# Performance work log

Measured on AMD Instinct MI355X. Metric: run time of the kernel, lower is better.

The kernel has to match this reference:

```python
import jax, jax.numpy as jnp
import numpy as np

B, N, D = 2, 2048, 1536
HEADS, KVH, DQK, DV = 8, 1, 128, 192
G = HEADS // KVH  # query groups per kv head
NP, DP = 512, 128  # pairwise seq len (coarse), pairwise feature dim
SCALE = DQK ** -0.5
CLAMP = 5.0
MOMENTUM = 0.1  # BatchRMSNorm: 1 - 0.9
EPS = 1e-5


def layernorm(x, w, b):
    mu = jnp.mean(x, axis=-1, keepdims=True)
    var = jnp.mean(jnp.square(x - mu), axis=-1, keepdims=True)
    return (x - mu) * jax.lax.rsqrt(var + EPS) * w + b


def setup_inputs() -> dict:
    key = jax.random.key(0)
    ks = jax.random.split(key, 6)
    w = lambda k, shape: jax.random.normal(k, shape, jnp.float32) * 0.02
    return {
        "x": jax.random.normal(ks[0], (B, N, D), jnp.float32),
        "pairwise": jax.random.normal(ks[1], (B, NP, NP, DP), jnp.float32),
        "w_qkv": w(ks[2], (D, HEADS * DQK + KVH * DQK + KVH * DV)),
        "q_w": jnp.ones((DQK,), jnp.float32), "q_b": jnp.zeros((DQK,), jnp.float32),
        "k_w": jnp.ones((DQK,), jnp.float32), "k_b": jnp.zeros((DQK,), jnp.float32),
        "v_w": jnp.ones((DV,), jnp.float32), "v_b": jnp.zeros((DV,), jnp.float32),
        "bias_gamma": jnp.ones((DP,), jnp.float32),
        "bias_beta": jnp.zeros((DP,), jnp.float32),
        "bias_running_var": jnp.ones((DP,), jnp.float32),
        "w_bias": w(ks[3], (DP, HEADS)),
        "w_out": w(ks[4], (HEADS * DV, D)),
        "b_out": jnp.zeros((D,), jnp.float32),
    }


def reference(x, pairwise, w_qkv, q_w, q_b, k_w, k_b, v_w, v_b,
              bias_gamma, bias_beta, bias_running_var, w_bias, w_out, b_out):
    b, n, _ = x.shape
    qkv = x @ w_qkv
    q, k, v = jnp.split(qkv, [HEADS * DQK, HEADS * DQK + KVH * DQK], axis=-1)
    # split heads: q -> b g h n d, k/v -> b h n d
    q = q.reshape(b, n, G, KVH, DQK).transpose(0, 2, 3, 1, 4)
    k = k.reshape(b, n, KVH, DQK).transpose(0, 2, 1, 3)
    v = v.reshape(b, n, KVH, DV).transpose(0, 2, 1, 3)
    q = layernorm(q, q_w, q_b)
    k = layernorm(k, k_w, k_b)
    v = layernorm(v, v_w, v_b)

    sim = jnp.einsum('bghid,bhjd->bghij', q, k) * SCALE

    # BatchRMSNorm (training update of running_var, then normalize)
    flat = pairwise.reshape(-1, DP)
    batch_var = jnp.var(flat, axis=0)  # unbiased=False
    rv = bias_running_var * (1.0 - MOMENTUM) + MOMENTUM * batch_var
    std = jnp.sqrt(rv + EPS)
    normed = pairwise / std * bias_gamma + bias_beta
    bias = jax.nn.gelu(normed, approximate=False) @ w_bias  # b i j (g h)
    bias = bias.reshape(b, NP, NP, G, KVH).transpose(0, 3, 4, 1, 2)  # b g h i j
    r = n // NP  # expand_factor
    bias = jnp.repeat(jnp.repeat(bias, r, axis=-2), r, axis=-1)

    sim = jnp.tanh((sim + bias) / CLAMP) * CLAMP  # softclamp
    attn = jax.nn.softmax(sim, axis=-1)
    out = jnp.einsum('bghij,bhjd->bghid', attn, v)
    out = out.transpose(0, 3, 1, 2, 4).reshape(b, n, HEADS * DV)  # merge heads
    return out @ w_out + b_out
```

## Files before the change

### kernel.cpp

```cpp
#include <hip/hip_runtime.h>
#include <math.h>

typedef _Float16 f16;
typedef unsigned int u32;
typedef __attribute__((ext_vector_type(8))) f16 f16x8;
typedef __attribute__((ext_vector_type(4))) f16 f16x4;
typedef __attribute__((ext_vector_type(4))) float f32x4;
typedef __attribute__((ext_vector_type(16))) float f32x16;

#define DEV static __device__ __forceinline__

#define SEQ 2048
#define DMODEL 1536
#define NHEADS 8
#define DQK 128
#define DVV 192
#define QKVW 1344
#define SCALEQK 0.08838834764831845f
#define LOG2E 1.4426950408889634f

#define OFF_WQKVT 0ull
#define OFF_WOUTT 4128768ull
#define OFF_XH    8847360ull
#define OFF_QKV   21430272ull
#define OFF_Q     43450368ull
#define OFF_K     51838976ull
#define OFF_V     52887552ull
#define OFF_VT    54460416ull
#define OFF_PART  56033280ull
#define OFF_SG    57081856ull
#define OFF_BIASC 57082880ull
#define OFF_AO    65471488ull

DEV float fexp2(float x){
#if __has_builtin(__builtin_amdgcn_exp2f)
  return __builtin_amdgcn_exp2f(x);
#else
  return exp2f(x);
#endif
}
DEV float frcp(float x){
#if __has_builtin(__builtin_amdgcn_rcpf)
  return __builtin_amdgcn_rcpf(x);
#else
  return 1.0f/x;
#endif
}

typedef u32 __attribute__((address_space(1))) u32g;
typedef u32 __attribute__((address_space(3))) u32l;
DEV void g2l16(const void* g, void* l){
  __builtin_amdgcn_global_load_lds((const u32g*)g, (u32l*)l, 16, 0, 0);
}

#define MFMA32(a,b,c) __builtin_amdgcn_mfma_f32_32x32x16_f16(a,b,c,0,0,0)
#define MFMA16(a,b,c) __builtin_amdgcn_mfma_f32_16x16x32_f16(a,b,c,0,0,0)

DEV f32x16 zero16(){
  f32x16 v;
  #pragma unroll
  for (int i=0;i<16;i++) v[i]=0.f;
  return v;
}
DEV f32x4 zero4(){
  f32x4 v;
  #pragma unroll
  for (int i=0;i<4;i++) v[i]=0.f;
  return v;
}

DEV float gelu_f(float x){
  float z  = 0.70710678118654752440f * x;
  float az = fabsf(z);
  float t  = frcp(1.f + 0.3275911f*az);
  float poly = t*(0.254829592f + t*(-0.284496736f + t*(1.421413741f +
               t*(-1.453152027f + t*1.061405429f))));
  float e  = 1.f - poly*fexp2(-z*z*LOG2E);
  float er = (z < 0.f) ? -e : e;
  return 0.5f*x*(1.f + er);
}

__global__ __launch_bounds__(256) void k1_prep(const float* __restrict__ wq, f16* __restrict__ wqT,
                                               const float* __restrict__ wo, f16* __restrict__ woT,
                                               const float* __restrict__ X, f16* __restrict__ Xh){
  __shared__ float t[32][33];
  int bid = blockIdx.x, tid = threadIdx.x;
  if (bid >= 4320){
    size_t i0 = (size_t)(bid - 4320)*2048 + (size_t)tid*8;
    f32x4 a = *(const f32x4*)(X + i0);
    f32x4 b = *(const f32x4*)(X + i0 + 4);
    f16x8 o;
    #pragma unroll
    for (int e=0;e<4;e++){ o[e] = (f16)a[e]; o[4+e] = (f16)b[e]; }
    *(f16x8*)(Xh + i0) = o;
    return;
  }
  int tx = tid & 31, ty = tid >> 5;
  const float* src; f16* dst; int N, x, y;
  if (bid < 2016){ src = wq; dst = wqT; N = 1344; x = bid % 48; y = bid / 48; }
  else { int b2 = bid - 2016; src = wo; dst = woT; N = 1536; x = b2 % 48; y = b2 / 48; }
  int k0 = x*32, n0 = y*32;
  #pragma unroll
  for (int i=0;i<4;i++){ int r = ty+8*i; t[r][tx] = src[(size_t)(k0+r)*N + n0+tx]; }
  __syncthreads();
  #pragma unroll
  for (int i=0;i<4;i++){ int r = ty+8*i; dst[(size_t)(n0+r)*1536 + k0+tx] = (f16)t[tx][r]; }
}

DEV void gemm256_body(const f16* __restrict__ A, const f16* __restrict__ WT,
                      float* __restrict__ C, int ldc, const float* __restrict__ bo,
                      char* lds, int bx, int by, int tid){
  int nb = bx*64, mb = by*256;
  int w = tid>>6, lane = tid&63, li = lane&31, h = lane>>5;
  int srow = lane>>3, sc = lane&7;
  f32x16 acc[2][2];
  acc[0][0]=zero16(); acc[0][1]=zero16(); acc[1][0]=zero16(); acc[1][1]=zero16();

#define G_STAGE(buf, kt_) do { \
    char* ad = lds + (buf)*40960; \
    _Pragma("unroll") \
    for (int s=0;s<8;s++){ \
      int slot = w*8+s; int mlr = slot*8 + srow; int cs = sc ^ (srow&7); \
      g2l16(A + (size_t)(mb+mlr)*DMODEL + (kt_)*64 + cs*8, ad + slot*1024); \
    } \
    char* bd = lds + (buf)*40960 + 32768; \
    _Pragma("unroll") \
    for (int s=0;s<2;s++){ \
      int slot = w*2+s; int nl = slot*8 + srow; int cs = sc ^ (srow&7); \
      g2l16(WT + (size_t)(nb+nl)*DMODEL + (kt_)*64 + cs*8, bd + slot*1024); \
    } } while(0)

  G_STAGE(0,0);
  __syncthreads();
  for (int kt=0; kt<24; kt++){
    int cur = kt&1;
    if (kt<23) G_STAGE(cur^1, kt+1);
    const char* ad = lds + cur*40960;
    const char* bd = lds + cur*40960 + 32768;
    #pragma unroll
    for (int ks=0; ks<4; ks++){
      int cso = ((2*ks+h) ^ (li&7))*16;
      f16x8 a0 = *(const f16x8*)(ad + (w*64      + li)*128 + cso);
      f16x8 a1 = *(const f16x8*)(ad + (w*64 + 32 + li)*128 + cso);
      f16x8 b0 = *(const f16x8*)(bd + (           li)*128 + cso);
      f16x8 b1 = *(const f16x8*)(bd + (      32 + li)*128 + cso);
      acc[0][0] = MFMA32(a0, b0, acc[0][0]);
      acc[0][1] = MFMA32(a0, b1, acc[0][1]);
      acc[1][0] = MFMA32(a1, b0, acc[1][0]);
      acc[1][1] = MFMA32(a1, b1, acc[1][1]);
    }
    __syncthreads();
  }
  float bo0 = bo ? bo[nb+li] : 0.f, bo1 = bo ? bo[nb+32+li] : 0.f;
  #pragma unroll
  for (int mi=0; mi<2; mi++)
    #pragma unroll
    for (int nf=0; nf<2; nf++)
      #pragma unroll
      for (int r=0;r<16;r++){
        int m = mb + w*64 + mi*32 + (r&3) + 8*(r>>2) + 4*h;
        int n = nb + nf*32 + li;
        C[(size_t)m*ldc + n] = acc[mi][nf][r] + (nf ? bo1 : bo0);
      }
#undef G_STAGE
}

DEV void pvar_body(const float* __restrict__ pw, float* __restrict__ partials,
                   char* smem, int id, int tid){
  int q = tid & 31, rg = tid >> 5;
  f32x4 s1 = zero4(), s2 = zero4();
  const float* p0 = pw + ((size_t)id*512 + rg)*128 + q*4;
  #pragma unroll 4
  for (int it=0; it<64; it++){
    f32x4 v = *(const f32x4*)(p0 + (size_t)it*1024);
    s1 += v; s2 += v*v;
  }
  f32x4* r1 = (f32x4*)smem; f32x4* r2 = r1 + 256;
  r1[tid] = s1; r2[tid] = s2;
  __syncthreads();
  if (tid < 64){
    int qq = tid & 31;
    f32x4* rr = (tid >= 32) ? r2 : r1;
    f32x4 a = rr[qq];
    #pragma unroll
    for (int g=1; g<8; g++) a += rr[g*32+qq];
    *(f32x4*)(partials + (size_t)id*256 + ((tid>=32)?128:0) + qq*4) = a;
  }
}

__global__ __launch_bounds__(256,2) void k2_qkv_pvar(const f16* __restrict__ Xh,
    const f16* __restrict__ WT, float* __restrict__ qkv,
    const float* __restrict__ pw, float* __restrict__ partials){
  __shared__ char smem[81920];
  int bid = blockIdx.x, tid = threadIdx.x;
  if (bid % 5 == 0){
    int qid = bid/5;
    int l = (qid&7)*42 + (qid>>3);
    gemm256_body(Xh, WT, qkv, QKVW, (const float*)0, smem, l%21, l/21, tid);
  } else {
    int pid = bid - bid/5 - 1;
    if (pid < 1024) pvar_body(pw, partials, smem, pid, tid);
  }
}

DEV void ln_unit(const float* __restrict__ qkv,
    const float* __restrict__ qw, const float* __restrict__ qb,
    const float* __restrict__ kw, const float* __restrict__ kb,
    const float* __restrict__ vw, const float* __restrict__ vb,
    f16* __restrict__ Q, f16* __restrict__ K, f16* __restrict__ V,
    int unit, int lane){
  int row = unit / 10, seg = unit - row*10;
  int b = row >> 11, n = row & 2047;
  const float* base = qkv + (size_t)row*QKVW;
  if (seg < 9){
    int off = seg*128;
    float x0 = base[off+lane], x1 = base[off+64+lane];
    float s = x0+x1;
    #pragma unroll
    for (int d=32; d>=1; d>>=1) s += __shfl_xor(s, d);
    float mu = s*(1.f/128.f);
    float d0 = x0-mu, d1 = x1-mu;
    float vv = d0*d0 + d1*d1;
    #pragma unroll
    for (int d=32; d>=1; d>>=1) vv += __shfl_xor(vv, d);
    float istd = rsqrtf(vv*(1.f/128.f) + 1e-5f);
    const float* W  = (seg<8)? qw : kw;
    const float* Bi = (seg<8)? qb : kb;
    f16* dst = (seg<8) ? (Q + ((size_t)(b*NHEADS+seg)*SEQ + n)*DQK)
                       : (K + ((size_t)(b*SEQ+n))*DQK);
    dst[lane]    = (f16)(d0*istd*W[lane] + Bi[lane]);
    dst[lane+64] = (f16)(d1*istd*W[lane+64] + Bi[lane+64]);
  } else {
    float x0 = base[1152+lane], x1 = base[1152+64+lane], x2 = base[1152+128+lane];
    float s = x0+x1+x2;
    #pragma unroll
    for (int d=32; d>=1; d>>=1) s += __shfl_xor(s, d);
    float mu = s*(1.f/192.f);
    float d0=x0-mu, d1=x1-mu, d2=x2-mu;
    float vv = d0*d0+d1*d1+d2*d2;
    #pragma unroll
    for (int d=32; d>=1; d>>=1) vv += __shfl_xor(vv, d);
    float istd = rsqrtf(vv*(1.f/192.f) + 1e-5f);
    f16* dst = V + (size_t)(b*SEQ+n)*DVV;
    dst[lane]     = (f16)(d0*istd*vw[lane] + vb[lane]);
    dst[lane+64]  = (f16)(d1*istd*vw[lane+64] + vb[lane+64]);
    dst[lane+128] = (f16)(d2*istd*vw[lane+128] + vb[lane+128]);
  }
}

__global__ __launch_bounds__(256,4) void k3_ln_finvar(const float* __restrict__ qkv,
    const float* __restrict__ qw, const float* __restrict__ qb,
    const float* __restrict__ kw, const float* __restrict__ kb,
    const float* __restrict__ vw, const float* __restrict__ vb,
    f16* __restrict__ Q, f16* __restrict__ K, f16* __restrict__ V,
    const float* __restrict__ partials, const float* __restrict__ rvar,
    const float* __restrict__ gamma, const float* __restrict__ beta,
    float* __restrict__ sg, float* __restrict__ sb){
  __shared__ float sh[256];
  int bid = blockIdx.x, tid = threadIdx.x;
  if (bid < 10240){
    ln_unit(qkv, qw,qb,kw,kb,vw,vb, Q,K,V, bid*4 + (tid>>6), tid&63);
  } else {
    int c = tid & 127, wh = tid >> 7;
    float acc = 0.f;
    #pragma unroll 8
    for (int i=0;i<1024;i++) acc += partials[i*256 + wh*128 + c];
    sh[tid] = acc;
    __syncthreads();
    if (tid < 128){
      float s1 = sh[tid], s2 = sh[tid+128];
      const float Minv = 1.f/524288.f;
      float m = s1*Minv;
      float var = s2*Minv - m*m;
      float rv = rvar[tid]*0.9f + 0.1f*var;
      sg[tid] = rsqrtf(rv + 1e-5f)*gamma[tid];
      sb[tid] = beta[tid];
    }
  }
}

DEV void bias_body(const float* __restrict__ pw,
    const float* __restrict__ sg, const float* __restrict__ sb,
    const float* __restrict__ wb, f16* __restrict__ biasc, int bias_id, int tid){
  int w = tid>>6, lane = tid&63;
  int il = lane&15, kg = lane>>4;
  f16x8 bw[4];
  float sgr[32], sbr[32];
  #pragma unroll
  for (int t=0;t<4;t++)
    #pragma unroll
    for (int e=0;e<8;e++){
      int k = t*32 + kg*8 + e;
      bw[t][e] = (f16)((il<8) ? wb[k*8 + il] : 0.f);
      sgr[t*8+e] = sg[k];
      sbr[t*8+e] = sb[k];
    }
  for (int it=0; it<8; it++){
    int tile = bias_id*4 + w + it*4096;
    size_t rg = (size_t)tile*16 + il;
    f32x4 acc = zero4();
    #pragma unroll
    for (int t=0;t<4;t++){
      const float* sp = pw + rg*128 + t*32 + kg*8;
      f32x4 v0 = *(const f32x4*)sp;
      f32x4 v1 = *(const f32x4*)(sp+4);
      f16x8 af;
      #pragma unroll
      for (int e=0;e<4;e++) af[e]   = (f16)gelu_f(v0[e]*sgr[t*8+e]   + sbr[t*8+e]);
      #pragma unroll
      for (int e=0;e<4;e++) af[4+e] = (f16)gelu_f(v1[e]*sgr[t*8+4+e] + sbr[t*8+4+e]);
      acc = MFMA16(af, bw[t], acc);
    }
    if (il < 8){
      #pragma unroll
      for (int r=0;r<4;r++){
        size_t rr = (size_t)tile*16 + kg*4 + r;
        int bb = (int)(rr >> 18);
        int rem = (int)(rr & 262143);
        int ii = rem >> 9, jj = rem & 511;
        biasc[(((size_t)(bb*8 + il)*512) + ii)*512 + jj] = (f16)acc[r];
      }
    }
  }
}

DEV void vtrans_body(const f16* __restrict__ V, f16* __restrict__ VT,
                     f16 (*t)[33], int id, int tid){
  int b = id / 384, rem = id - b*384;
  int d0 = (rem % 6)*32, j0 = (rem / 6)*32;
  int tx = tid & 31, ty = tid >> 5;
  #pragma unroll
  for (int i=0;i<4;i++){ int r = ty+8*i; t[r][tx] = V[((size_t)b*SEQ + j0+r)*DVV + d0+tx]; }
  __syncthreads();
  #pragma unroll
  for (int i=0;i<4;i++){ int r = ty+8*i; VT[((size_t)b*DVV + d0+r)*SEQ + j0+tx] = t[tx][r]; }
}

__global__ __launch_bounds__(256,2) void k4_bias_vtrans(const float* __restrict__ pw,
    const float* __restrict__ sg, const float* __restrict__ sb,
    const float* __restrict__ wb, f16* __restrict__ biasc,
    const f16* __restrict__ V, f16* __restrict__ VT){
  __shared__ f16 tt[32][33];
  int bid = blockIdx.x, tid = threadIdx.x;
  if (bid < 1536){
    if (bid & 1) bias_body(pw, sg, sb, wb, biasc, bid>>1, tid);
    else         vtrans_body(V, VT, tt, bid>>1, tid);
  } else {
    bias_body(pw, sg, sb, wb, biasc, 768 + (bid - 1536), tid);
  }
}

__global__ __launch_bounds__(256,1) void attn(const f16* __restrict__ Q, const f16* __restrict__ K,
                                              const f16* __restrict__ VT, const f16* __restrict__ biasc,
                                              f16* __restrict__ AO){
  __shared__ char lds[81920];
  int bid = blockIdx.x;
  int bg = bid & 15, qt = bid >> 4;
  int b = bg >> 3, g = bg & 7;
  int tid = threadIdx.x;
  int w = tid >> 6, lane = tid & 63;
  int li = lane & 31, h = lane >> 5;

  const f16* Qb = Q  + (size_t)bg*SEQ*DQK;
  const f16* Kb = K  + (size_t)b*SEQ*DQK;
  const f16* Vb = VT + (size_t)b*DVV*SEQ;

  int qrow = qt*128 + w*32 + li;
  f16x8 qf[8];
  #pragma unroll
  for (int ks=0; ks<8; ks++)
    qf[ks] = *(const f16x8*)(Qb + (size_t)qrow*DQK + ks*16 + h*8);

  const f16* brow = biasc + ((size_t)bg*512 + (qrow>>2))*512;

  f32x16 oacc[6];
  #pragma unroll
  for (int nf=0;nf<6;nf++) oacc[nf] = zero16();
  float lsum = 0.f;

  int kl_row = lane >> 4, kl_c = lane & 15;
  int vl_row = lane >> 3, vl_c = lane & 7;

#define STAGE(buf, jt_) do { \
    char* kd = lds + (buf)*40960; \
    const f16* ksrc = Kb + (size_t)(jt_)*64*DQK; \
    _Pragma("unroll") \
    for (int s=0;s<4;s++){ \
      int slot = w*4+s; int jr = slot*4 + kl_row; int cs = kl_c ^ (jr&7); \
      g2l16(ksrc + (size_t)jr*DQK + cs*8, kd + slot*1024); \
    } \
    char* vd = lds + (buf)*40960 + 16384; \
    _Pragma("unroll") \
    for (int s=0;s<6;s++){ \
      int slot = w*6+s; int dvr = slot*8 + vl_row; int cs = vl_c ^ (dvr&7); \
      g2l16(Vb + (size_t)dvr*SEQ + (size_t)(jt_)*64 + cs*8, vd + slot*1024); \
    } } while(0)

  STAGE(0, 0);

  const float CS = SCALEQK * (2.f*LOG2E/5.f);
  const float CB = 2.f*LOG2E/5.f;
  const float CP = 5.f*LOG2E;

  for (int jt=0; jt<32; jt++){
    int cur = jt & 1;
    __syncthreads();
    if (jt < 31) STAGE(cur^1, jt+1);
    const char* kb_ = lds + cur*40960;
    const char* vb_ = lds + cur*40960 + 16384;

    f32x16 s0 = zero16(), s1 = zero16();
    #pragma unroll
    for (int ks=0; ks<8; ks++){
      int cso = ((2*ks + h) ^ (li&7))*16;
      f16x8 kf0 = *(const f16x8*)(kb_ + (     li)*256 + cso);
      f16x8 kf1 = *(const f16x8*)(kb_ + (32 + li)*256 + cso);
      s0 = MFMA32(kf0, qf[ks], s0);
      s1 = MFMA32(kf1, qf[ks], s1);
    }

    f16x8 pa[2][2];
    #pragma unroll
    for (int sub=0; sub<2; sub++){
      const f32x16& sacc = sub ? s1 : s0;
      int jb4 = jt*16 + sub*8;
      f16x8 bv = *(const f16x8*)(brow + jb4);
      float bt[4];
      #pragma unroll
      for (int q=0;q<4;q++){
        float b0 = (float)bv[2*q], b1 = (float)bv[2*q+1];
        bt[q] = (h ? b1 : b0) * CB;
      }
      float p[16], xp[16];
      #pragma unroll
      for (int r=0;r<16;r++){
        float u2 = sacc[r]*CS + bt[r>>2];
        float E  = fexp2(u2);
        float tn = 1.f - 2.f*frcp(E + 1.f);
        float pr = fexp2(tn * CP);
        p[r] = pr;
        lsum += pr;
      }
      #pragma unroll
      for (int r=0;r<16;r++) xp[r] = __shfl_xor(p[r], 32);
      #pragma unroll
      for (int ks2=0; ks2<2; ks2++){
        #pragma unroll
        for (int e=0;e<4;e++) pa[sub][ks2][e] = (f16)(h ? xp[8*ks2+4+e] : p[8*ks2+e]);
        #pragma unroll
        for (int e=4;e<8;e++) pa[sub][ks2][e] = (f16)(h ? p[8*ks2+e]    : xp[8*ks2+e-4]);
      }
    }
    #pragma unroll
    for (int sub=0; sub<2; sub++)
      #pragma unroll
      for (int ks2=0; ks2<2; ks2++)
        #pragma unroll
        for (int nf=0; nf<6; nf++){
          int dvr = nf*32 + li;
          int cj = (sub*4 + 2*ks2 + h) ^ (dvr&7);
          f16x8 vf = *(const f16x8*)(vb_ + dvr*128 + cj*16);
          oacc[nf] = MFMA32(pa[sub][ks2], vf, oacc[nf]);
        }
  }
  float ltot = lsum + __shfl_xor(lsum, 32);
  float linv = 1.f / ltot;
  #pragma unroll
  for (int nf=0; nf<6; nf++)
    #pragma unroll
    for (int r=0;r<16;r++){
      int il = (r&3) + 8*(r>>2) + 4*h;
      float ov = oacc[nf][r] * __shfl(linv, il);
      int orow = qt*128 + w*32 + il;
      AO[((size_t)(b*SEQ + orow)*NHEADS + g)*DVV + nf*32 + li] = (f16)ov;
    }
#undef STAGE
}

__global__ __launch_bounds__(256,2) void out_gemm(const f16* __restrict__ A, const f16* __restrict__ WT,
                                                  const float* __restrict__ bo, float* __restrict__ out){
  __shared__ char lds[81920];
  int bid = blockIdx.x, tid = threadIdx.x;
  int l = (bid&7)*48 + (bid>>3);
  gemm256_body(A, WT, out, DMODEL, bo, lds, l%24, l/24, tid);
}

extern "C" void kernel_launch(void* const* d_in, const int* in_sizes, int n_in,
                              void* d_out, int out_size, void* d_ws, size_t ws_size,
                              hipStream_t stream) {
  (void)in_sizes; (void)n_in; (void)out_size; (void)ws_size;
  const float* x        = (const float*)d_in[0];
  const float* pairwise = (const float*)d_in[1];
  const float* w_qkv    = (const float*)d_in[2];
  const float* q_w      = (const float*)d_in[3];
  const float* q_b      = (const float*)d_in[4];
  const float* k_w      = (const float*)d_in[5];
  const float* k_b      = (const float*)d_in[6];
  const float* v_w      = (const float*)d_in[7];
  const float* v_b      = (const float*)d_in[8];
  const float* bgamma   = (const float*)d_in[9];
  const float* bbeta    = (const float*)d_in[10];
  const float* brvar    = (const float*)d_in[11];
  const float* w_bias   = (const float*)d_in[12];
  const float* w_out    = (const float*)d_in[13];
  const float* b_out    = (const float*)d_in[14];
  float* out = (float*)d_out;

  char* ws = (char*)d_ws;
  f16*   wqkvT = (f16*)(ws + OFF_WQKVT);
  f16*   woutT = (f16*)(ws + OFF_WOUTT);
  f16*   Xh    = (f16*)(ws + OFF_XH);
  float* qkvb  = (float*)(ws + OFF_QKV);
  f16*   Qh    = (f16*)(ws + OFF_Q);
  f16*   Kh    = (f16*)(ws + OFF_K);
  f16*   Vh    = (f16*)(ws + OFF_V);
  f16*   VTh   = (f16*)(ws + OFF_VT);
  float* part  = (float*)(ws + OFF_PART);
  float* sg    = (float*)(ws + OFF_SG);
  float* sb    = sg + 128;
  f16*   biasc = (f16*)(ws + OFF_BIASC);
  f16*   AOh   = (f16*)(ws + OFF_AO);

  k1_prep<<<7392, 256, 0, stream>>>(w_qkv, wqkvT, w_out, woutT, x, Xh);
  k2_qkv_pvar<<<1680, 256, 0, stream>>>(Xh, wqkvT, qkvb, pairwise, part);
  k3_ln_finvar<<<10241, 256, 0, stream>>>(qkvb, q_w,q_b,k_w,k_b,v_w,v_b, Qh, Kh, Vh,
                                          part, brvar, bgamma, bbeta, sg, sb);
  k4_bias_vtrans<<<1792, 256, 0, stream>>>(pairwise, sg, sb, w_bias, biasc, Vh, VTh);
  attn<<<256, 256, 0, stream>>>(Qh, Kh, VTh, biasc, AOh);
  out_gemm<<<384, 256, 0, stream>>>(AOh, woutT, b_out, out);
}
```

Measured before the change: 358.6 us.

## Split attention key range across two blocks and combine partial outputs

Each attention block now processes half of the key tiles, doubling the grid and allowing two blocks per CU. Unnormalized fp32 partial outputs and row sums are written to workspace, and a new combine kernel adds them, normalizes, and writes fp16 output. No max rescaling is needed because the softclamp bounds scores. This trades extra global memory traffic and a kernel launch for better occupancy and latency hiding.

Measured after the change: 337.6 us. -5.9%, faster.

```diff
diff --git a/kernel.cpp b/kernel.cpp
--- a/kernel.cpp
+++ b/kernel.cpp
@@ -31,6 +31,8 @@
 #define OFF_SG    57081856ull
 #define OFF_BIASC 57082880ull
 #define OFF_AO    65471488ull
+#define OFF_OP    78054400ull
+#define OFF_LS    128386048ull
 
 DEV float fexp2(float x){
 #if __has_builtin(__builtin_amdgcn_exp2f)
@@ -350,13 +352,14 @@
   }
 }
 
-__global__ __launch_bounds__(256,1) void attn(const f16* __restrict__ Q, const f16* __restrict__ K,
+__global__ __launch_bounds__(256,2) void attn(const f16* __restrict__ Q, const f16* __restrict__ K,
                                               const f16* __restrict__ VT, const f16* __restrict__ biasc,
-                                              f16* __restrict__ AO){
+                                              float* __restrict__ Opart, float* __restrict__ Ls){
   __shared__ char lds[81920];
   int bid = blockIdx.x;
-  int bg = bid & 15, qt = bid >> 4;
-  int b = bg >> 3, g = bg & 7;
+  int half = bid & 1, bgqt = bid >> 1;
+  int bg = bgqt & 15, qt = bgqt >> 4;
+  int b = bg >> 3;
   int tid = threadIdx.x;
   int w = tid >> 6, lane = tid & 63;
   int li = lane & 31, h = lane >> 5;
@@ -396,16 +399,18 @@
       g2l16(Vb + (size_t)dvr*SEQ + (size_t)(jt_)*64 + cs*8, vd + slot*1024); \
     } } while(0)
 
-  STAGE(0, 0);
+  int jt0 = half*16;
+  STAGE(0, jt0);
 
   const float CS = SCALEQK * (2.f*LOG2E/5.f);
   const float CB = 2.f*LOG2E/5.f;
   const float CP = 5.f*LOG2E;
 
-  for (int jt=0; jt<32; jt++){
-    int cur = jt & 1;
+  for (int jj=0; jj<16; jj++){
+    int jt = jt0 + jj;
+    int cur = jj & 1;
     __syncthreads();
-    if (jt < 31) STAGE(cur^1, jt+1);
+    if (jj < 15) STAGE(cur^1, jt+1);
     const char* kb_ = lds + cur*40960;
     const char* vb_ = lds + cur*40960 + 16384;
 
@@ -463,18 +468,44 @@
           oacc[nf] = MFMA32(pa[sub][ks2], vf, oacc[nf]);
         }
   }
-  float ltot = lsum + __shfl_xor(lsum, 32);
-  float linv = 1.f / ltot;
+  float* Ob = Opart + (size_t)(bgqt*2 + half)*128*192;
   #pragma unroll
   for (int nf=0; nf<6; nf++)
     #pragma unroll
     for (int r=0;r<16;r++){
       int il = (r&3) + 8*(r>>2) + 4*h;
-      float ov = oacc[nf][r] * __shfl(linv, il);
-      int orow = qt*128 + w*32 + il;
-      AO[((size_t)(b*SEQ + orow)*NHEADS + g)*DVV + nf*32 + li] = (f16)ov;
-    }
+      Ob[(size_t)(w*32 + il)*192 + nf*32 + li] = oacc[nf][r];
+    }
+  float ltot = lsum + __shfl_xor(lsum, 32);
+  if (h == 0) Ls[(size_t)(bgqt*2 + half)*128 + w*32 + li] = ltot;
 #undef STAGE
+}
+
+__global__ __launch_bounds__(256) void attn_combine(const float* __restrict__ Opart,
+                                                    const float* __restrict__ Ls,
+                                                    f16* __restrict__ AO){
+  int tid = threadIdx.x;
+  int pr = blockIdx.x*16 + (tid>>4);
+  int sub = tid & 15;
+  int bgqt = pr >> 7, row = pr & 127;
+  int bg = bgqt & 15, qt = bgqt >> 4;
+  int b = bg >> 3, g = bg & 7;
+  int n = qt*128 + row;
+  float l0 = Ls[(size_t)(bgqt*2 + 0)*128 + row];
+  float l1 = Ls[(size_t)(bgqt*2 + 1)*128 + row];
+  float linv = 1.f / (l0 + l1);
+  const float* O0 = Opart + ((size_t)(bgqt*2 + 0)*128 + row)*192 + sub*12;
+  const float* O1 = Opart + ((size_t)(bgqt*2 + 1)*128 + row)*192 + sub*12;
+  f16* dst = AO + ((size_t)(b*SEQ + n)*NHEADS + g)*DVV + sub*12;
+  #pragma unroll
+  for (int j=0;j<3;j++){
+    f32x4 a = *(const f32x4*)(O0 + 4*j);
+    f32x4 c = *(const f32x4*)(O1 + 4*j);
+    f16x4 o;
+    #pragma unroll
+    for (int e=0;e<4;e++) o[e] = (f16)((a[e] + c[e]) * linv);
+    *(f16x4*)(dst + 4*j) = o;
+  }
 }
 
 __global__ __launch_bounds__(256,2) void out_gemm(const f16* __restrict__ A, const f16* __restrict__ WT,
@@ -520,12 +551,15 @@
   float* sb    = sg + 128;
   f16*   biasc = (f16*)(ws + OFF_BIASC);
   f16*   AOh   = (f16*)(ws + OFF_AO);
+  float* Opart = (float*)(ws + OFF_OP);
+  float* Lsw   = (float*)(ws + OFF_LS);
 
   k1_prep<<<7392, 256, 0, stream>>>(w_qkv, wqkvT, w_out, woutT, x, Xh);
   k2_qkv_pvar<<<1680, 256, 0, stream>>>(Xh, wqkvT, qkvb, pairwise, part);
   k3_ln_finvar<<<10241, 256, 0, stream>>>(qkvb, q_w,q_b,k_w,k_b,v_w,v_b, Qh, Kh, Vh,
                                           part, brvar, bgamma, bbeta, sg, sb);
   k4_bias_vtrans<<<1792, 256, 0, stream>>>(pairwise, sg, sb, w_bias, biasc, Vh, VTh);
-  attn<<<256, 256, 0, stream>>>(Qh, Kh, VTh, biasc, AOh);
+  attn<<<512, 256, 0, stream>>>(Qh, Kh, VTh, biasc, Opart, Lsw);
+  attn_combine<<<2048, 256, 0, stream>>>(Opart, Lsw, AOh);
   out_gemm<<<384, 256, 0, stream>>>(AOh, woutT, b_out, out);
 }
```
